# Performance work log

Hardware: AMD Instinct MI355X
Metric: run time of the kernel (lower is better)

## Reference

```python
import jax, jax.numpy as jnp
import numpy as np

BUCKET_SIZE = 64
N_HASHES = 8
EPS = 1e-6
SELF_MASK_VAL = -1e5


def setup_inputs() -> dict:
    key = jax.random.key(0)
    k1, k2, k3 = jax.random.split(key, 3)
    B, S, D = 8, 4096, 128
    n_buckets = S // BUCKET_SIZE  # 64, even as required
    qk = jax.random.normal(k1, (B, S, D), dtype=jnp.float32)
    v = jax.random.normal(k2, (B, S, D), dtype=jnp.float32)
    # shared random rotations (random_rotations_per_head=False): (dim, n_hashes, n_buckets//2)
    rotations = jax.random.normal(k3, (D, N_HASHES, n_buckets // 2), dtype=jnp.float32)
    return {"qk": qk, "v": v, "rotations": rotations}


def _look_one_back(x):
    # prepend previous chunk (with wraparound) along the key/value axis
    x_extra = jnp.concatenate([x[:, -1:], x[:, :-1]], axis=1)
    return jnp.concatenate([x, x_extra], axis=2)


def reference(qk, v, rotations):
    B, S, D = qk.shape
    n_buckets = S // BUCKET_SIZE
    n_bins = n_buckets
    C = N_HASHES * n_bins  # number of chunks per sequence (chunk size = BUCKET_SIZE)

    # --- hash_vectors ---
    rot = jnp.einsum('btf,fhi->bhti', qk, rotations)          # [B,H,S,nb/2]
    rot = jnp.concatenate([rot, -rot], axis=-1)               # [B,H,S,nb]
    buckets = jnp.argmax(rot, axis=-1)                        # [B,H,S]
    offsets = (jnp.arange(N_HASHES) * n_buckets).reshape(1, -1, 1)
    buckets = (buckets + offsets).reshape(B, -1)              # [B, H*S]

    # --- sort tokens by (bucket, position) ---
    ticker = jnp.arange(N_HASHES * S)[None, :]
    buckets_and_t = S * buckets + (ticker % S)                # unique keys
    sticker = jnp.argsort(buckets_and_t, axis=-1)             # [B, H*S]
    undo_sort = jnpp_argsort = jnp.argsort(sticker, axis=-1)
    st = sticker % S

    sqk = jnp.take_along_axis(qk, st[..., None], axis=1)      # [B,H*S,D]
    sv = jnp.take_along_axis(v, st[..., None], axis=1)

    bq_t = st.reshape(B, C, -1)                               # [B,C,chunk]
    bqk = sqk.reshape(B, C, -1, D)
    bv = sv.reshape(B, C, -1, D)

    bq = bqk
    bk = bqk * jax.lax.rsqrt(jnp.sum(bqk * bqk, axis=-1, keepdims=True) + EPS)

    bk = _look_one_back(bk)                                   # [B,C,2*chunk,D]
    bv = _look_one_back(bv)
    bkv_t = _look_one_back(bq_t)

    dots = jnp.einsum('bcie,bcje->bcij', bq, bk) * (D ** -0.5)
    self_mask = bq_t[:, :, :, None] == bkv_t[:, :, None, :]
    dots = jnp.where(self_mask, SELF_MASK_VAL, dots)

    lse = jax.nn.logsumexp(dots, axis=-1, keepdims=True)
    probs = jnp.exp(dots - lse)
    bo = jnp.einsum('bcij,bcje->bcie', probs, bv)             # [B,C,chunk,D]

    so = bo.reshape(B, -1, D)                                 # [B,H*S,D]
    slogits = lse.reshape(B, -1)                              # [B,H*S]

    # unsort
    o = jnp.take_along_axis(so, undo_sort[..., None], axis=1)
    logits = jnp.take_along_axis(slogits, undo_sort, axis=1)

    # combine the n_hashes rounds with softmax over per-round logsumexp
    o = o.reshape(B, N_HASHES, S, D)
    logits = logits.reshape(B, N_HASHES, S, 1)
    w = jnp.exp(logits - jax.nn.logsumexp(logits, axis=1, keepdims=True))
    out = jnp.sum(o * w, axis=1)                              # [B,S,D]
    return out, buckets
```

## Files before the change

### kernel.cpp

```cpp
#include <hip/hip_runtime.h>
#include <hip/hip_bf16.h>

#define BB 8
#define SS 4096
#define DD 128
#define HH 8
#define NBUCK 64
#define CHUNKSZ 64
#define NCHUNK 512
#define HSTOT 32768
#define ROWB 272

typedef __attribute__((ext_vector_type(8))) short short8_t;
typedef __attribute__((ext_vector_type(4))) float f32x4;

static __device__ __forceinline__ unsigned short f2bf(float f) {
    __hip_bfloat16 h = __float2bfloat16(f);
    return *reinterpret_cast<unsigned short*>(&h);
}
static __device__ __forceinline__ unsigned int pk2bf(float lo, float hi) {
    __hip_bfloat162 h = __float22bfloat162_rn(make_float2(lo, hi));
    return *reinterpret_cast<unsigned int*>(&h);
}
static __device__ __forceinline__ float bf2f(unsigned short u) {
    return __uint_as_float(((unsigned int)u) << 16);
}

__global__ __launch_bounds__(256) void hash_kernel(
    const float* __restrict__ qk, const float* __restrict__ rot,
    unsigned char* __restrict__ bucket_ws, float* __restrict__ bucket_out)
{
    const int tid = threadIdx.x;
    const int bid = blockIdx.x;
    const int b   = bid & 7;
    const int h   = (bid >> 3) & 7;
    const int t0  = (bid >> 6) * 128;
    const int tg  = tid >> 3;
    const int jq  = tid & 7;

    const float* qbase = qk + ((size_t)b * SS + t0 + tg * 4) * DD;
    const float* rbase = rot + h * 32 + jq * 4;

    float acc[4][4];
    #pragma unroll
    for (int r = 0; r < 4; ++r)
        #pragma unroll
        for (int j = 0; j < 4; ++j) acc[r][j] = 0.f;

    for (int c = 0; c < 16; ++c) {
        float4 qv[4][2];
        #pragma unroll
        for (int r = 0; r < 4; ++r) {
            qv[r][0] = *reinterpret_cast<const float4*>(qbase + r * DD + c * 8);
            qv[r][1] = *reinterpret_cast<const float4*>(qbase + r * DD + c * 8 + 4);
        }
        float4 rv[8];
        #pragma unroll
        for (int ff = 0; ff < 8; ++ff)
            rv[ff] = *reinterpret_cast<const float4*>(rbase + (size_t)(c * 8 + ff) * (HH * 32));
        #pragma unroll
        for (int ff = 0; ff < 8; ++ff) {
            #pragma unroll
            for (int r = 0; r < 4; ++r) {
                const float4 qh = qv[r][ff >> 2];
                const float qs = (ff & 2) ? ((ff & 1) ? qh.w : qh.z)
                                          : ((ff & 1) ? qh.y : qh.x);
                acc[r][0] = fmaf(qs, rv[ff].x, acc[r][0]);
                acc[r][1] = fmaf(qs, rv[ff].y, acc[r][1]);
                acc[r][2] = fmaf(qs, rv[ff].z, acc[r][2]);
                acc[r][3] = fmaf(qs, rv[ff].w, acc[r][3]);
            }
        }
    }

    const float TAU = 0.01f;
    #pragma unroll
    for (int r = 0; r < 4; ++r) {
        float bv = -3.0e38f; int bi = 0;
        #pragma unroll
        for (int j = 0; j < 4; ++j) {
            float v = acc[r][j];
            if (v > bv) { bv = v; bi = jq * 4 + j; }
        }
        #pragma unroll
        for (int j = 0; j < 4; ++j) {
            float v = -acc[r][j];
            if (v > bv) { bv = v; bi = 32 + jq * 4 + j; }
        }
        #pragma unroll
        for (int off = 1; off < 8; off <<= 1) {
            float ov = __shfl_xor(bv, off);
            int   oi = __shfl_xor(bi, off);
            if (ov > bv || (ov == bv && oi < bi)) { bv = ov; bi = oi; }
        }
        const float thrv = bv - TAU;
        int cnt = 0;
        #pragma unroll
        for (int j = 0; j < 4; ++j) {
            cnt += (acc[r][j]  > thrv) ? 1 : 0;
            cnt += (-acc[r][j] > thrv) ? 1 : 0;
        }
        #pragma unroll
        for (int off = 1; off < 8; off <<= 1) cnt += __shfl_xor(cnt, off);

        const int t = t0 + tg * 4 + r;
        if (cnt > 1) {
            const float* qrow = qk + ((size_t)b * SS + t) * DD;
            double bvd = -1.0e300; int bid2 = 64;
            #pragma unroll
            for (int j = 0; j < 4; ++j) {
                const bool fp = (acc[r][j] > thrv);
                const bool fn = (-acc[r][j] > thrv);
                if (fp || fn) {
                    const float* rcol = rot + h * 32 + jq * 4 + j;
                    double a = 0.0;
                    for (int f = 0; f < DD; ++f)
                        a = fma((double)qrow[f], (double)rcol[(size_t)f * (HH * 32)], a);
                    if (fp &&  a > bvd)                         { bvd = a;  bid2 = jq * 4 + j; }
                    if (fn && (-a > bvd ||
                               (-a == bvd && 32 + jq * 4 + j < bid2))) { bvd = -a; bid2 = 32 + jq * 4 + j; }
                }
            }
            #pragma unroll
            for (int off = 1; off < 8; off <<= 1) {
                double ov = __shfl_xor(bvd, off);
                int    oi = __shfl_xor(bid2, off);
                if (ov > bvd || (ov == bvd && oi < bid2)) { bvd = ov; bid2 = oi; }
            }
            bi = bid2;
        }
        if (jq == 0) {
            const size_t o = ((size_t)b * HH + h) * SS + t;
            bucket_ws[o]  = (unsigned char)bi;
            bucket_out[o] = (float)(bi + h * NBUCK);
        }
    }
}

__global__ __launch_bounds__(256) void sort_kernel(
    const unsigned char* __restrict__ bucket_ws, int* __restrict__ st)
{
    __shared__ unsigned int hist[256 * 65];
    __shared__ unsigned int totals[64];
    const int tid = threadIdx.x;
    const int bh  = blockIdx.x;

    unsigned int* hrow = &hist[tid * 65];
    #pragma unroll
    for (int j = 0; j < 65; ++j) hrow[j] = 0u;

    const uint4 raw = *reinterpret_cast<const uint4*>(bucket_ws + (size_t)bh * SS + tid * 16);
    unsigned int w[4] = {raw.x, raw.y, raw.z, raw.w};

    #pragma unroll
    for (int c = 0; c < 16; ++c) {
        unsigned int bk = (w[c >> 2] >> ((c & 3) * 8)) & 255u;
        hrow[bk] += 1u;
    }
    __syncthreads();

    if (tid < 64) {
        unsigned int run = 0;
        for (int c2 = 0; c2 < 256; ++c2) {
            unsigned int x = hist[c2 * 65 + tid];
            hist[c2 * 65 + tid] = run;
            run += x;
        }
        totals[tid] = run;
    }
    __syncthreads();
    if (tid == 0) {
        unsigned int base = 0;
        for (int k = 0; k < 64; ++k) { unsigned int x = totals[k]; totals[k] = base; base += x; }
    }
    __syncthreads();

    int* dst = st + (size_t)bh * SS;
    #pragma unroll
    for (int c = 0; c < 16; ++c) {
        unsigned int bk = (w[c >> 2] >> ((c & 3) * 8)) & 255u;
        unsigned int pos = totals[bk] + hrow[bk];
        hrow[bk] += 1u;
        dst[pos] = tid * 16 + c;
    }
}

__global__ __launch_bounds__(256, 4) void attn_kernel(
    const float* __restrict__ qk, const float* __restrict__ vv,
    const int* __restrict__ st, float* __restrict__ logits_ws,
    void* __restrict__ o_ws, const int obf16)
{
    __shared__ __align__(16) char smem[36864];
    char*  Kb    = smem;
    char*  Pb    = smem;
    char*  Vt    = smem + 17408;
    int*   tks   = (int*)(smem + 34816);
    float* ninv  = (float*)(smem + 35328);
    float* psums = (float*)(smem + 35840);

    const int tid = threadIdx.x;
    const int bc  = blockIdx.x;
    const int b   = bc & 7;
    const int c   = bc >> 3;
    const int h   = c >> 6;

    const int rowk  = tid >> 1, halfk = tid & 1;
    const int src_r = (rowk < 64) ? c : ((c == 0) ? (NCHUNK - 1) : (c - 1));
    const int t_mine = st[(size_t)b * HSTOT + (size_t)src_r * CHUNKSZ + (rowk & 63)];

    if (tid < 128) {
        int src_c = (tid < 64) ? c : ((c == 0) ? (NCHUNK - 1) : (c - 1));
        tks[tid] = st[(size_t)b * HSTOT + (size_t)src_c * CHUNKSZ + (tid & 63)];
    }

    {
        const float* srow = qk + ((size_t)b * SS + t_mine) * DD + halfk * 64;
        char* krow = Kb + (size_t)rowk * ROWB + halfk * 128;
        float ss = 0.f;
        #pragma unroll
        for (int i = 0; i < 8; ++i) {
            float4 v0 = *reinterpret_cast<const float4*>(srow + i * 8);
            float4 v1 = *reinterpret_cast<const float4*>(srow + i * 8 + 4);
            ss = fmaf(v0.x, v0.x, ss); ss = fmaf(v0.y, v0.y, ss);
            ss = fmaf(v0.z, v0.z, ss); ss = fmaf(v0.w, v0.w, ss);
            ss = fmaf(v1.x, v1.x, ss); ss = fmaf(v1.y, v1.y, ss);
            ss = fmaf(v1.z, v1.z, ss); ss = fmaf(v1.w, v1.w, ss);
            uint4 pk;
            pk.x = pk2bf(v0.x, v0.y); pk.y = pk2bf(v0.z, v0.w);
            pk.z = pk2bf(v1.x, v1.y); pk.w = pk2bf(v1.z, v1.w);
            *reinterpret_cast<uint4*>(krow + i * 16) = pk;
        }
        psums[tid] = ss;
    }
    __syncthreads();
    if (tid < 128) ninv[tid] = rsqrtf(psums[2 * tid] + psums[2 * tid + 1] + 1e-6f);
    __syncthreads();

    const int w  = tid >> 6;
    const int ln = tid & 63;
    const int cc = ln & 15;
    const int g  = ln >> 4;

    short8_t aq[4];
    #pragma unroll
    for (int ks = 0; ks < 4; ++ks)
        aq[ks] = *reinterpret_cast<const short8_t*>(Kb + (size_t)(16 * w + cc) * ROWB + ks * 64 + g * 16);

    f32x4 acc[8];
    __builtin_amdgcn_s_setprio(1);
    #pragma unroll
    for (int j = 0; j < 8; ++j) {
        acc[j] = (f32x4){0.f, 0.f, 0.f, 0.f};
        #pragma unroll
        for (int ks = 0; ks < 4; ++ks) {
            short8_t bk = *reinterpret_cast<const short8_t*>(Kb + (size_t)(16 * j + cc) * ROWB + ks * 64 + g * 16);
            acc[j] = __builtin_amdgcn_mfma_f32_16x16x32_bf16(aq[ks], bk, acc[j], 0, 0, 0);
        }
    }
    __builtin_amdgcn_s_setprio(0);

    const float SCALE = 0.088388347648318447f;
    float lse[4];
    float pr[8][4];
    #pragma unroll
    for (int jr = 0; jr < 4; ++jr) {
        const int q  = 16 * w + 4 * g + jr;
        const int tq = tks[q];
        float m = -3.0e38f;
        #pragma unroll
        for (int j = 0; j < 8; ++j) {
            const int k = 16 * j + cc;
            float val = acc[j][jr] * (ninv[k] * SCALE);
            if (tks[k] == tq) val = -1e5f;
            pr[j][jr] = val;
            m = fmaxf(m, val);
        }
        #pragma unroll
        for (int off = 1; off < 16; off <<= 1) m = fmaxf(m, __shfl_xor(m, off));
        float ssum = 0.f;
        #pragma unroll
        for (int j = 0; j < 8; ++j) { float ex = expf(pr[j][jr] - m); pr[j][jr] = ex; ssum += ex; }
        #pragma unroll
        for (int off = 1; off < 16; off <<= 1) ssum += __shfl_xor(ssum, off);
        const float inv = 1.0f / ssum;
        #pragma unroll
        for (int j = 0; j < 8; ++j) pr[j][jr] *= inv;
        lse[jr] = m + logf(ssum);
    }

    const int kp = tid & 63;
    const int db = tid >> 6;
    const int tva = tks[2 * kp], tvb = tks[2 * kp + 1];
    const float* vra = vv + ((size_t)b * SS + tva) * DD + db * 16;
    const float* vrb = vv + ((size_t)b * SS + tvb) * DD + db * 16;
    float4 va[4], vbr[4];
    #pragma unroll
    for (int i = 0; i < 4; ++i) {
        va[i]  = *reinterpret_cast<const float4*>(vra + i * 4);
        vbr[i] = *reinterpret_cast<const float4*>(vrb + i * 4);
    }

    __syncthreads();

    #pragma unroll
    for (int jr = 0; jr < 4; ++jr) {
        const int q = 16 * w + 4 * g + jr;
        #pragma unroll
        for (int j = 0; j < 8; ++j)
            *reinterpret_cast<unsigned short*>(Pb + (size_t)q * ROWB + (16 * j + cc) * 2) = f2bf(pr[j][jr]);
    }
    if (cc == 0) {
        #pragma unroll
        for (int jr = 0; jr < 4; ++jr) {
            const int q = 16 * w + 4 * g + jr;
            logits_ws[((size_t)b * HH + h) * SS + tks[q]] = lse[jr];
        }
    }
    {
        const float* fa = reinterpret_cast<const float*>(va);
        const float* fb = reinterpret_cast<const float*>(vbr);
        #pragma unroll
        for (int i = 0; i < 16; ++i) {
            const int dl = db * 16 + i;
            *reinterpret_cast<unsigned int*>(Vt + (size_t)dl * ROWB + kp * 4) = pk2bf(fa[i], fb[i]);
        }
    }
    #pragma unroll
    for (int i = 0; i < 4; ++i) {
        va[i]  = *reinterpret_cast<const float4*>(vra + 64 + i * 4);
        vbr[i] = *reinterpret_cast<const float4*>(vrb + 64 + i * 4);
    }
    __syncthreads();

    short8_t pa[4];
    #pragma unroll
    for (int ks = 0; ks < 4; ++ks)
        pa[ks] = *reinterpret_cast<const short8_t*>(Pb + (size_t)(16 * w + cc) * ROWB + ks * 64 + g * 16);

    f32x4 oacc[8];
    __builtin_amdgcn_s_setprio(1);
    #pragma unroll
    for (int dt = 0; dt < 4; ++dt) {
        oacc[dt] = (f32x4){0.f, 0.f, 0.f, 0.f};
        #pragma unroll
        for (int ks = 0; ks < 4; ++ks) {
            short8_t vb = *reinterpret_cast<const short8_t*>(Vt + (size_t)(16 * dt + cc) * ROWB + ks * 64 + g * 16);
            oacc[dt] = __builtin_amdgcn_mfma_f32_16x16x32_bf16(pa[ks], vb, oacc[dt], 0, 0, 0);
        }
    }
    __builtin_amdgcn_s_setprio(0);
    __syncthreads();

    {
        const float* fa = reinterpret_cast<const float*>(va);
        const float* fb = reinterpret_cast<const float*>(vbr);
        #pragma unroll
        for (int i = 0; i < 16; ++i) {
            const int dl = db * 16 + i;
            *reinterpret_cast<unsigned int*>(Vt + (size_t)dl * ROWB + kp * 4) = pk2bf(fa[i], fb[i]);
        }
    }
    __syncthreads();

    __builtin_amdgcn_s_setprio(1);
    #pragma unroll
    for (int dt = 4; dt < 8; ++dt) {
        oacc[dt] = (f32x4){0.f, 0.f, 0.f, 0.f};
        #pragma unroll
        for (int ks = 0; ks < 4; ++ks) {
            short8_t vb = *reinterpret_cast<const short8_t*>(Vt + (size_t)(16 * (dt - 4) + cc) * ROWB + ks * 64 + g * 16);
            oacc[dt] = __builtin_amdgcn_mfma_f32_16x16x32_bf16(pa[ks], vb, oacc[dt], 0, 0, 0);
        }
    }
    __builtin_amdgcn_s_setprio(0);

    #pragma unroll
    for (int jr = 0; jr < 4; ++jr) {
        const int q = 16 * w + 4 * g + jr;
        const int t = tks[q];
        const size_t base = (((size_t)b * HH + h) * SS + t) * DD + cc;
        if (!obf16) {
            float* op = (float*)o_ws;
            #pragma unroll
            for (int dt = 0; dt < 8; ++dt) op[base + 16 * dt] = oacc[dt][jr];
        } else {
            unsigned short* op = (unsigned short*)o_ws;
            #pragma unroll
            for (int dt = 0; dt < 8; ++dt) op[base + 16 * dt] = f2bf(oacc[dt][jr]);
        }
    }
}

__global__ __launch_bounds__(256) void combine_kernel(
    const float* __restrict__ logits_ws, const void* __restrict__ o_ws,
    float* __restrict__ outp, const int obf16)
{
    const int gid = blockIdx.x * 256 + threadIdx.x;
    const int row = gid >> 5;
    const int seg = gid & 31;
    const int b = row >> 12;
    const int t = row & 4095;

    float l[8];
    float m = -3.0e38f;
    #pragma unroll
    for (int hh = 0; hh < 8; ++hh) {
        l[hh] = logits_ws[((size_t)b * HH + hh) * SS + t];
        m = fmaxf(m, l[hh]);
    }
    float ssum = 0.f;
    #pragma unroll
    for (int hh = 0; hh < 8; ++hh) { l[hh] = expf(l[hh] - m); ssum += l[hh]; }
    const float inv = 1.0f / ssum;

    float a0 = 0.f, a1 = 0.f, a2 = 0.f, a3 = 0.f;
    #pragma unroll
    for (int hh = 0; hh < 8; ++hh) {
        const float wgt = l[hh] * inv;
        const size_t base = (((size_t)b * HH + hh) * SS + t) * DD + seg * 4;
        if (!obf16) {
            float4 ov = *reinterpret_cast<const float4*>((const float*)o_ws + base);
            a0 = fmaf(wgt, ov.x, a0); a1 = fmaf(wgt, ov.y, a1);
            a2 = fmaf(wgt, ov.z, a2); a3 = fmaf(wgt, ov.w, a3);
        } else {
            uint2 u = *reinterpret_cast<const uint2*>((const unsigned short*)o_ws + base);
            a0 = fmaf(wgt, bf2f((unsigned short)(u.x & 0xffffu)), a0);
            a1 = fmaf(wgt, bf2f((unsigned short)(u.x >> 16)), a1);
            a2 = fmaf(wgt, bf2f((unsigned short)(u.y & 0xffffu)), a2);
            a3 = fmaf(wgt, bf2f((unsigned short)(u.y >> 16)), a3);
        }
    }
    *reinterpret_cast<float4*>(outp + ((size_t)b * SS + t) * DD + seg * 4) =
        make_float4(a0, a1, a2, a3);
}

extern "C" void kernel_launch(void* const* d_in, const int* in_sizes, int n_in,
                              void* d_out, int out_size, void* d_ws, size_t ws_size,
                              hipStream_t stream) {
    const float* qk  = (const float*)d_in[0];
    const float* v   = (const float*)d_in[1];
    const float* rot = (const float*)d_in[2];

    float* out        = (float*)d_out;
    float* bucket_out = out + (size_t)BB * SS * DD;

    char* ws = (char*)d_ws;
    int*            st        = (int*)ws;
    unsigned char*  bucket_ws = (unsigned char*)(ws + 1048576);
    float*          logits_ws = (float*)(ws + 1048576 + 262144);
    void*           o_ws      = (void*)(ws + 2359296);

    const int obf16 = 1;

    hipLaunchKernelGGL(hash_kernel,    dim3(2048), dim3(256), 0, stream, qk, rot, bucket_ws, bucket_out);
    hipLaunchKernelGGL(sort_kernel,    dim3(64),   dim3(256), 0, stream, bucket_ws, st);
    hipLaunchKernelGGL(attn_kernel,    dim3(4096), dim3(256), 0, stream, qk, v, st, logits_ws, o_ws, obf16);
    hipLaunchKernelGGL(combine_kernel, dim3(4096), dim3(256), 0, stream, logits_ws, o_ws, out, obf16);
}
```

Baseline: 179.4 us.

## Precompute key norms in hash kernel, swizzle LDS layout, drop LDS index tables

```diff
diff --git a/kernel.cpp b/kernel.cpp
--- a/kernel.cpp
+++ b/kernel.cpp
@@ -9,7 +9,8 @@
 #define CHUNKSZ 64
 #define NCHUNK 512
 #define HSTOT 32768
-#define ROWB 272
+#define ROWB 256
+#define SWZ(row, off) ((off) ^ (((row) & 7) << 4))
 
 typedef __attribute__((ext_vector_type(8))) short short8_t;
 typedef __attribute__((ext_vector_type(4))) float f32x4;
@@ -28,7 +29,8 @@
 
 __global__ __launch_bounds__(256) void hash_kernel(
     const float* __restrict__ qk, const float* __restrict__ rot,
-    unsigned char* __restrict__ bucket_ws, float* __restrict__ bucket_out)
+    unsigned char* __restrict__ bucket_ws, float* __restrict__ bucket_out,
+    float* __restrict__ ninv_ws)
 {
     const int tid = threadIdx.x;
     const int bid = blockIdx.x;
@@ -42,6 +44,7 @@
     const float* rbase = rot + h * 32 + jq * 4;
 
     float acc[4][4];
+    float ssq[4] = {0.f, 0.f, 0.f, 0.f};
     #pragma unroll
     for (int r = 0; r < 4; ++r)
         #pragma unroll
@@ -53,6 +56,18 @@
         for (int r = 0; r < 4; ++r) {
             qv[r][0] = *reinterpret_cast<const float4*>(qbase + r * DD + c * 8);
             qv[r][1] = *reinterpret_cast<const float4*>(qbase + r * DD + c * 8 + 4);
+        }
+        if (h == 0) {
+            #pragma unroll
+            for (int r = 0; r < 4; ++r) {
+                float4 a0 = qv[r][0], a1 = qv[r][1];
+                float s = ssq[r];
+                s = fmaf(a0.x, a0.x, s); s = fmaf(a0.y, a0.y, s);
+                s = fmaf(a0.z, a0.z, s); s = fmaf(a0.w, a0.w, s);
+                s = fmaf(a1.x, a1.x, s); s = fmaf(a1.y, a1.y, s);
+                s = fmaf(a1.z, a1.z, s); s = fmaf(a1.w, a1.w, s);
+                ssq[r] = s;
+            }
         }
         float4 rv[8];
         #pragma unroll
@@ -71,6 +86,12 @@
                 acc[r][3] = fmaf(qs, rv[ff].w, acc[r][3]);
             }
         }
+    }
+
+    if (h == 0 && jq == 0) {
+        #pragma unroll
+        for (int r = 0; r < 4; ++r)
+            ninv_ws[(size_t)b * SS + t0 + tg * 4 + r] = rsqrtf(ssq[r] + 1e-6f);
     }
 
     const float TAU = 0.01f;
@@ -185,66 +206,71 @@
     }
 }
 
-__global__ __launch_bounds__(256, 4) void attn_kernel(
+__global__ __launch_bounds__(256, 5) void attn_kernel(
     const float* __restrict__ qk, const float* __restrict__ vv,
-    const int* __restrict__ st, float* __restrict__ logits_ws,
-    void* __restrict__ o_ws, const int obf16)
+    const int* __restrict__ st, const float* __restrict__ ninv_ws,
+    float* __restrict__ logits_ws, void* __restrict__ o_ws, const int obf16)
 {
-    __shared__ __align__(16) char smem[36864];
-    char*  Kb    = smem;
-    char*  Pb    = smem;
-    char*  Vt    = smem + 17408;
-    int*   tks   = (int*)(smem + 34816);
-    float* ninv  = (float*)(smem + 35328);
-    float* psums = (float*)(smem + 35840);
+    __shared__ __align__(16) char smem[32768];
+    char*  Kb = smem;
+    char*  Pb = smem;
+    char*  Vt = smem + 16384;
 
     const int tid = threadIdx.x;
     const int bc  = blockIdx.x;
     const int b   = bc & 7;
     const int c   = bc >> 3;
     const int h   = c >> 6;
+    const int cprev = (c == 0) ? (NCHUNK - 1) : (c - 1);
+    const int* stb  = st + (size_t)b * HSTOT;
 
     const int rowk  = tid >> 1, halfk = tid & 1;
-    const int src_r = (rowk < 64) ? c : ((c == 0) ? (NCHUNK - 1) : (c - 1));
-    const int t_mine = st[(size_t)b * HSTOT + (size_t)src_r * CHUNKSZ + (rowk & 63)];
-
-    if (tid < 128) {
-        int src_c = (tid < 64) ? c : ((c == 0) ? (NCHUNK - 1) : (c - 1));
-        tks[tid] = st[(size_t)b * HSTOT + (size_t)src_c * CHUNKSZ + (tid & 63)];
-    }
-
-    {
-        const float* srow = qk + ((size_t)b * SS + t_mine) * DD + halfk * 64;
-        char* krow = Kb + (size_t)rowk * ROWB + halfk * 128;
-        float ss = 0.f;
-        #pragma unroll
-        for (int i = 0; i < 8; ++i) {
-            float4 v0 = *reinterpret_cast<const float4*>(srow + i * 8);
-            float4 v1 = *reinterpret_cast<const float4*>(srow + i * 8 + 4);
-            ss = fmaf(v0.x, v0.x, ss); ss = fmaf(v0.y, v0.y, ss);
-            ss = fmaf(v0.z, v0.z, ss); ss = fmaf(v0.w, v0.w, ss);
-            ss = fmaf(v1.x, v1.x, ss); ss = fmaf(v1.y, v1.y, ss);
-            ss = fmaf(v1.z, v1.z, ss); ss = fmaf(v1.w, v1.w, ss);
-            uint4 pk;
-            pk.x = pk2bf(v0.x, v0.y); pk.y = pk2bf(v0.z, v0.w);
-            pk.z = pk2bf(v1.x, v1.y); pk.w = pk2bf(v1.z, v1.w);
-            *reinterpret_cast<uint4*>(krow + i * 16) = pk;
-        }
-        psums[tid] = ss;
-    }
-    __syncthreads();
-    if (tid < 128) ninv[tid] = rsqrtf(psums[2 * tid] + psums[2 * tid + 1] + 1e-6f);
-    __syncthreads();
+    const int t_mine = stb[(size_t)((rowk < 64) ? c : cprev) * CHUNKSZ + (rowk & 63)];
 
     const int w  = tid >> 6;
     const int ln = tid & 63;
     const int cc = ln & 15;
     const int g  = ln >> 4;
+    const int kp = tid & 63;
+    const int db = tid >> 6;
+
+    int tks_k[8]; float ninv_r[8];
+    #pragma unroll
+    for (int j = 0; j < 8; ++j) {
+        const int idx = 16 * j + cc;
+        const int tk  = stb[(size_t)((idx < 64) ? c : cprev) * CHUNKSZ + (idx & 63)];
+        tks_k[j] = tk;
+        ninv_r[j] = ninv_ws[(size_t)b * SS + tk];
+    }
+    int tq[4];
+    #pragma unroll
+    for (int jr = 0; jr < 4; ++jr)
+        tq[jr] = stb[(size_t)c * CHUNKSZ + (16 * w + 4 * g + jr)];
+    const int idxa = 2 * kp, idxb = 2 * kp + 1;
+    const int tva = stb[(size_t)((idxa < 64) ? c : cprev) * CHUNKSZ + (idxa & 63)];
+    const int tvb = stb[(size_t)((idxb < 64) ? c : cprev) * CHUNKSZ + (idxb & 63)];
+
+    {
+        const float* srow = qk + ((size_t)b * SS + t_mine) * DD + halfk * 64;
+        char* krow = Kb + (size_t)rowk * ROWB;
+        #pragma unroll
+        for (int i = 0; i < 8; ++i) {
+            float4 v0 = *reinterpret_cast<const float4*>(srow + i * 8);
+            float4 v1 = *reinterpret_cast<const float4*>(srow + i * 8 + 4);
+            uint4 pk;
+            pk.x = pk2bf(v0.x, v0.y); pk.y = pk2bf(v0.z, v0.w);
+            pk.z = pk2bf(v1.x, v1.y); pk.w = pk2bf(v1.z, v1.w);
+            *reinterpret_cast<uint4*>(krow + SWZ(rowk, halfk * 128 + i * 16)) = pk;
+        }
+    }
+    __syncthreads();
 
     short8_t aq[4];
     #pragma unroll
-    for (int ks = 0; ks < 4; ++ks)
-        aq[ks] = *reinterpret_cast<const short8_t*>(Kb + (size_t)(16 * w + cc) * ROWB + ks * 64 + g * 16);
+    for (int ks = 0; ks < 4; ++ks) {
+        const int row = 16 * w + cc;
+        aq[ks] = *reinterpret_cast<const short8_t*>(Kb + (size_t)row * ROWB + SWZ(row, ks * 64 + g * 16));
+    }
 
     f32x4 acc[8];
     __builtin_amdgcn_s_setprio(1);
@@ -253,7 +279,8 @@
         acc[j] = (f32x4){0.f, 0.f, 0.f, 0.f};
         #pragma unroll
         for (int ks = 0; ks < 4; ++ks) {
-            short8_t bk = *reinterpret_cast<const short8_t*>(Kb + (size_t)(16 * j + cc) * ROWB + ks * 64 + g * 16);
+            const int row = 16 * j + cc;
+            short8_t bk = *reinterpret_cast<const short8_t*>(Kb + (size_t)row * ROWB + SWZ(row, ks * 64 + g * 16));
             acc[j] = __builtin_amdgcn_mfma_f32_16x16x32_bf16(aq[ks], bk, acc[j], 0, 0, 0);
         }
     }
@@ -264,14 +291,11 @@
     float pr[8][4];
     #pragma unroll
     for (int jr = 0; jr < 4; ++jr) {
-        const int q  = 16 * w + 4 * g + jr;
-        const int tq = tks[q];
         float m = -3.0e38f;
         #pragma unroll
         for (int j = 0; j < 8; ++j) {
-            const int k = 16 * j + cc;
-            float val = acc[j][jr] * (ninv[k] * SCALE);
-            if (tks[k] == tq) val = -1e5f;
+            float val = acc[j][jr] * (ninv_r[j] * SCALE);
+            if (tks_k[j] == tq[jr]) val = -1e5f;
             pr[j][jr] = val;
             m = fmaxf(m, val);
         }
@@ -288,9 +312,6 @@
         lse[jr] = m + logf(ssum);
     }
 
-    const int kp = tid & 63;
-    const int db = tid >> 6;
-    const int tva = tks[2 * kp], tvb = tks[2 * kp + 1];
     const float* vra = vv + ((size_t)b * SS + tva) * DD + db * 16;
     const float* vrb = vv + ((size_t)b * SS + tvb) * DD + db * 16;
     float4 va[4], vbr[4];
@@ -307,14 +328,12 @@
         const int q = 16 * w + 4 * g + jr;
         #pragma unroll
         for (int j = 0; j < 8; ++j)
-            *reinterpret_cast<unsigned short*>(Pb + (size_t)q * ROWB + (16 * j + cc) * 2) = f2bf(pr[j][jr]);
+            *reinterpret_cast<unsigned short*>(Pb + (size_t)q * ROWB + SWZ(q, (16 * j + cc) * 2)) = f2bf(pr[j][jr]);
     }
     if (cc == 0) {
         #pragma unroll
-        for (int jr = 0; jr < 4; ++jr) {
-            const int q = 16 * w + 4 * g + jr;
-            logits_ws[((size_t)b * HH + h) * SS + tks[q]] = lse[jr];
-        }
+        for (int jr = 0; jr < 4; ++jr)
+            logits_ws[((size_t)b * HH + h) * SS + tq[jr]] = lse[jr];
     }
     {
         const float* fa = reinterpret_cast<const float*>(va);
@@ -322,7 +341,7 @@
         #pragma unroll
         for (int i = 0; i < 16; ++i) {
             const int dl = db * 16 + i;
-            *reinterpret_cast<unsigned int*>(Vt + (size_t)dl * ROWB + kp * 4) = pk2bf(fa[i], fb[i]);
+            *reinterpret_cast<unsigned int*>(Vt + (size_t)dl * ROWB + SWZ(dl, kp * 4)) = pk2bf(fa[i], fb[i]);
         }
     }
     #pragma unroll
@@ -334,8 +353,10 @@
 
     short8_t pa[4];
     #pragma unroll
-    for (int ks = 0; ks < 4; ++ks)
-        pa[ks] = *reinterpret_cast<const short8_t*>(Pb + (size_t)(16 * w + cc) * ROWB + ks * 64 + g * 16);
+    for (int ks = 0; ks < 4; ++ks) {
+        const int row = 16 * w + cc;
+        pa[ks] = *reinterpret_cast<const short8_t*>(Pb + (size_t)row * ROWB + SWZ(row, ks * 64 + g * 16));
+    }
 
     f32x4 oacc[8];
     __builtin_amdgcn_s_setprio(1);
@@ -344,7 +365,8 @@
         oacc[dt] = (f32x4){0.f, 0.f, 0.f, 0.f};
         #pragma unroll
         for (int ks = 0; ks < 4; ++ks) {
-            short8_t vb = *reinterpret_cast<const short8_t*>(Vt + (size_t)(16 * dt + cc) * ROWB + ks * 64 + g * 16);
+            const int row = 16 * dt + cc;
+            short8_t vb = *reinterpret_cast<const short8_t*>(Vt + (size_t)row * ROWB + SWZ(row, ks * 64 + g * 16));
             oacc[dt] = __builtin_amdgcn_mfma_f32_16x16x32_bf16(pa[ks], vb, oacc[dt], 0, 0, 0);
         }
     }
@@ -357,7 +379,7 @@
         #pragma unroll
         for (int i = 0; i < 16; ++i) {
             const int dl = db * 16 + i;
-            *reinterpret_cast<unsigned int*>(Vt + (size_t)dl * ROWB + kp * 4) = pk2bf(fa[i], fb[i]);
+            *reinterpret_cast<unsigned int*>(Vt + (size_t)dl * ROWB + SWZ(dl, kp * 4)) = pk2bf(fa[i], fb[i]);
         }
     }
     __syncthreads();
@@ -368,7 +390,8 @@
         oacc[dt] = (f32x4){0.f, 0.f, 0.f, 0.f};
         #pragma unroll
         for (int ks = 0; ks < 4; ++ks) {
-            short8_t vb = *reinterpret_cast<const short8_t*>(Vt + (size_t)(16 * (dt - 4) + cc) * ROWB + ks * 64 + g * 16);
+            const int row = 16 * (dt - 4) + cc;
+            short8_t vb = *reinterpret_cast<const short8_t*>(Vt + (size_t)row * ROWB + SWZ(row, ks * 64 + g * 16));
             oacc[dt] = __builtin_amdgcn_mfma_f32_16x16x32_bf16(pa[ks], vb, oacc[dt], 0, 0, 0);
         }
     }
@@ -376,8 +399,7 @@
 
     #pragma unroll
     for (int jr = 0; jr < 4; ++jr) {
-        const int q = 16 * w + 4 * g + jr;
-        const int t = tks[q];
+        const int t = tq[jr];
         const size_t base = (((size_t)b * HH + h) * SS + t) * DD + cc;
         if (!obf16) {
             float* op = (float*)o_ws;
@@ -448,12 +470,13 @@
     int*            st        = (int*)ws;
     unsigned char*  bucket_ws = (unsigned char*)(ws + 1048576);
     float*          logits_ws = (float*)(ws + 1048576 + 262144);
-    void*           o_ws      = (void*)(ws + 2359296);
+    float*          ninv_ws   = (float*)(ws + 2359296);
+    void*           o_ws      = (void*)(ws + 2490368);
 
     const int obf16 = 1;
 
-    hipLaunchKernelGGL(hash_kernel,    dim3(2048), dim3(256), 0, stream, qk, rot, bucket_ws, bucket_out);
+    hipLaunchKernelGGL(hash_kernel,    dim3(2048), dim3(256), 0, stream, qk, rot, bucket_ws, bucket_out, ninv_ws);
     hipLaunchKernelGGL(sort_kernel,    dim3(64),   dim3(256), 0, stream, bucket_ws, st);
-    hipLaunchKernelGGL(attn_kernel,    dim3(4096), dim3(256), 0, stream, qk, v, st, logits_ws, o_ws, obf16);
+    hipLaunchKernelGGL(attn_kernel,    dim3(4096), dim3(256), 0, stream, qk, v, st, ninv_ws, logits_ws, o_ws, obf16);
     hipLaunchKernelGGL(combine_kernel, dim3(4096), dim3(256), 0, stream, logits_ws, o_ws, out, obf16);
 }
```

Result: slower. 206.2 us (+14.9%).
